# Kernel optimization log

Hardware: AMD Instinct MI355X
Metric: run time of the kernel (lower is better)

The kernel has to match this reference:

```python
import jax, jax.numpy as jnp
import numpy as np

N_MED = 100000   # len(medicine_it): nodes in the single hyperedge
VOCAB = 200000   # medicine vocab (rows of both embedding tables)
C_IN = 256
C_OUT = 256


def setup_inputs() -> dict:
    key = jax.random.key(0)
    k1, k2, k3, k4, k5 = jax.random.split(key, 5)
    return {
        "medicine_it": jax.random.randint(k1, (N_MED,), 0, VOCAB),
        "m_embeddings": jax.random.normal(k2, (VOCAB, C_IN), dtype=jnp.float32),
        "pretrained_weight": jax.random.normal(k3, (VOCAB, C_OUT), dtype=jnp.float32),
        "W": jax.random.normal(k4, (C_OUT, C_IN), dtype=jnp.float32) / np.sqrt(C_IN).astype(np.float32),
        "bias": jax.random.normal(k5, (C_OUT,), dtype=jnp.float32) * 0.01,
    }


def reference(medicine_it, m_embeddings, pretrained_weight, W, bias):
    # --- forward(): gather medicine rows, HypergraphConv with ONE hyperedge ---
    x = m_embeddings[medicine_it]                 # [N, C_in]  row gather
    xw = x @ W.T                                  # [N, C_out] lin (bias added after propagation, as in PyG)
    n = xw.shape[0]
    # Single hyperedge containing all N nodes: edge degree B = N, node degree D = 1.
    # edge_feat = B^{-1} H^T (X W^T);  node_out = D^{-1} H edge_feat + bias (same for all nodes)
    edge_feat = jnp.sum(xw, axis=0) / jnp.asarray(n, xw.dtype)   # [C_out]
    med_node_feature = edge_feat[None, :] + bias                 # [1, C_out], identical per node
    # --- output(): sum_i pretrained[m_i] + sum_i representation[i] ---
    embedding_pretrained = jnp.sum(pretrained_weight[medicine_it], axis=0, keepdims=True)  # [1, C_out]
    embedding_trained = jnp.asarray(n, xw.dtype) * med_node_feature                        # [1, C_out]
    return (embedding_pretrained + embedding_trained)[None, :, :]  # [1, 1, C_out]
```

## Files before the change

kernel.cpp:

```cpp
#include <hip/hip_runtime.h>


#define NCOPY 16

__device__ inline void fma4(float4& acc, float w, const float4& v) {
    acc.x = fmaf(w, v.x, acc.x);
    acc.y = fmaf(w, v.y, acc.y);
    acc.z = fmaf(w, v.z, acc.z);
    acc.w = fmaf(w, v.w, acc.w);
}

__global__ __launch_bounds__(256) void hist_kernel(
    const int* __restrict__ idx, int* __restrict__ counts, int n)
{
    int i = blockIdx.x * blockDim.x + threadIdx.x;
    const int stride = gridDim.x * blockDim.x;
    for (; i < n; i += stride) atomicAdd(&counts[idx[i]], 1);
}

__global__ __launch_bounds__(256) void scan_kernel(
    const int* __restrict__ counts,
    const float* __restrict__ memb,
    const float* __restrict__ pre,
    float* __restrict__ acc,
    int vocab)
{
    const int lane = threadIdx.x & 63;
    const int wid  = (blockIdx.x * blockDim.x + threadIdx.x) >> 6;
    const int base = wid * 64;

    float4 accS = make_float4(0.f, 0.f, 0.f, 0.f);
    float4 accP = make_float4(0.f, 0.f, 0.f, 0.f);

    if (base < vocab) {
        int c = 0;
        if (base + lane < vocab) c = counts[base + lane];
        const float cf = (float)c;
        unsigned long long m = __ballot(c != 0);

        while (m) {
            const int k1 = __ffsll(m) - 1;  m &= m - 1;
            const float w1 = __shfl(cf, k1, 64);
            const float4 a1 = reinterpret_cast<const float4*>(memb + (size_t)(base + k1) * 256)[lane];
            const float4 b1 = reinterpret_cast<const float4*>(pre  + (size_t)(base + k1) * 256)[lane];
            if (m) {
                const int k2 = __ffsll(m) - 1;  m &= m - 1;
                const float w2 = __shfl(cf, k2, 64);
                const float4 a2 = reinterpret_cast<const float4*>(memb + (size_t)(base + k2) * 256)[lane];
                const float4 b2 = reinterpret_cast<const float4*>(pre  + (size_t)(base + k2) * 256)[lane];
                fma4(accS, w1, a1); fma4(accP, w1, b1);
                fma4(accS, w2, a2); fma4(accP, w2, b2);
            } else {
                fma4(accS, w1, a1); fma4(accP, w1, b1);
            }
        }
    }

    __shared__ float sS[256];
    __shared__ float sP[256];
    sS[threadIdx.x] = 0.f;
    sP[threadIdx.x] = 0.f;
    __syncthreads();

    const int ch = lane * 4;
    atomicAdd(&sS[ch + 0], accS.x); atomicAdd(&sS[ch + 1], accS.y);
    atomicAdd(&sS[ch + 2], accS.z); atomicAdd(&sS[ch + 3], accS.w);
    atomicAdd(&sP[ch + 0], accP.x); atomicAdd(&sP[ch + 1], accP.y);
    atomicAdd(&sP[ch + 2], accP.z); atomicAdd(&sP[ch + 3], accP.w);
    __syncthreads();

    float* myacc = acc + (size_t)(blockIdx.x & (NCOPY - 1)) * 512;
    atomicAdd(&myacc[threadIdx.x],       sS[threadIdx.x]);
    atomicAdd(&myacc[256 + threadIdx.x], sP[threadIdx.x]);
}

__global__ __launch_bounds__(256) void gather_sum_kernel(
    const int* __restrict__ idx,
    const float* __restrict__ memb,
    const float* __restrict__ pre,
    float* __restrict__ acc,
    int n)
{
    const int lane = threadIdx.x & 63;
    const int wave = threadIdx.x >> 6;
    const int globalWave = blockIdx.x * 4 + wave;
    const int totalWaves = gridDim.x * 4;

    float4 accS = make_float4(0.f, 0.f, 0.f, 0.f);
    float4 accP = make_float4(0.f, 0.f, 0.f, 0.f);

    for (int i = globalWave; i < n; i += totalWaves) {
        const int r = idx[i];
        const float4 a = reinterpret_cast<const float4*>(memb + (size_t)r * 256)[lane];
        const float4 b = reinterpret_cast<const float4*>(pre  + (size_t)r * 256)[lane];
        accS.x += a.x; accS.y += a.y; accS.z += a.z; accS.w += a.w;
        accP.x += b.x; accP.y += b.y; accP.z += b.z; accP.w += b.w;
    }

    __shared__ float sS[256];
    __shared__ float sP[256];
    sS[threadIdx.x] = 0.f;
    sP[threadIdx.x] = 0.f;
    __syncthreads();
    const int ch = lane * 4;
    atomicAdd(&sS[ch + 0], accS.x); atomicAdd(&sS[ch + 1], accS.y);
    atomicAdd(&sS[ch + 2], accS.z); atomicAdd(&sS[ch + 3], accS.w);
    atomicAdd(&sP[ch + 0], accP.x); atomicAdd(&sP[ch + 1], accP.y);
    atomicAdd(&sP[ch + 2], accP.z); atomicAdd(&sP[ch + 3], accP.w);
    __syncthreads();
    float* myacc = acc + (size_t)(blockIdx.x & (NCOPY - 1)) * 512;
    atomicAdd(&myacc[threadIdx.x],       sS[threadIdx.x]);
    atomicAdd(&myacc[256 + threadIdx.x], sP[threadIdx.x]);
}

__global__ __launch_bounds__(256) void finish_kernel(
    const float* __restrict__ acc,
    const float* __restrict__ W,
    const float* __restrict__ bias,
    float* __restrict__ out,
    float nf)
{
    const int c = blockIdx.x;
    const int t = threadIdx.x;

    float s_t = 0.f;
    #pragma unroll
    for (int cp = 0; cp < NCOPY; ++cp) s_t += acc[cp * 512 + t];

    float v = W[(size_t)c * 256 + t] * s_t;
    for (int off = 32; off > 0; off >>= 1)
        v += __shfl_down(v, off, 64);

    __shared__ float part[4];
    if ((t & 63) == 0) part[t >> 6] = v;
    __syncthreads();

    if (t == 0) {
        float p_c = 0.f;
        #pragma unroll
        for (int cp = 0; cp < NCOPY; ++cp) p_c += acc[cp * 512 + 256 + c];
        out[c] = (part[0] + part[1] + part[2] + part[3]) + p_c + nf * bias[c];
    }
}

extern "C" void kernel_launch(void* const* d_in, const int* in_sizes, int n_in,
                              void* d_out, int out_size, void* d_ws, size_t ws_size,
                              hipStream_t stream)
{
    const int*   idx  = (const int*)d_in[0];
    const float* memb = (const float*)d_in[1];
    const float* pre  = (const float*)d_in[2];
    const float* W    = (const float*)d_in[3];
    const float* bias = (const float*)d_in[4];
    float* out = (float*)d_out;

    const int n     = in_sizes[0];
    const int vocab = in_sizes[1] / 256;

    const size_t countsBytes = (size_t)vocab * sizeof(int);
    const size_t accBytes    = (size_t)NCOPY * 512 * sizeof(float);

    if (ws_size >= countsBytes + accBytes) {
        int*   counts = (int*)d_ws;
        float* acc    = (float*)((char*)d_ws + countsBytes);

        hipMemsetAsync(d_ws, 0, countsBytes + accBytes, stream);
        hist_kernel<<<400, 256, 0, stream>>>(idx, counts, n);

        const int waves  = (vocab + 63) / 64;
        const int blocks = (waves + 3) / 4;
        scan_kernel<<<blocks, 256, 0, stream>>>(counts, memb, pre, acc, vocab);
        finish_kernel<<<256, 256, 0, stream>>>(acc, W, bias, out, (float)n);
    } else {
        float* acc = (float*)d_ws;
        hipMemsetAsync(d_ws, 0, accBytes, stream);
        gather_sum_kernel<<<512, 256, 0, stream>>>(idx, memb, pre, acc, n);
        finish_kernel<<<256, 256, 0, stream>>>(acc, W, bias, out, (float)n);
    }
}
```

Measured before the change: 53.89 us.

## Fuse finish into scan via last-block pattern and compact nonzero rows in LDS

```diff
diff --git a/kernel.cpp b/kernel.cpp
--- a/kernel.cpp
+++ b/kernel.cpp
@@ -1,59 +1,61 @@
 #include <hip/hip_runtime.h>
 
 
+typedef float f4 __attribute__((ext_vector_type(4)));
+
 #define NCOPY 16
-
-__device__ inline void fma4(float4& acc, float w, const float4& v) {
-    acc.x = fmaf(w, v.x, acc.x);
-    acc.y = fmaf(w, v.y, acc.y);
-    acc.z = fmaf(w, v.z, acc.z);
-    acc.w = fmaf(w, v.w, acc.w);
-}
 
 __global__ __launch_bounds__(256) void hist_kernel(
     const int* __restrict__ idx, int* __restrict__ counts, int n)
 {
-    int i = blockIdx.x * blockDim.x + threadIdx.x;
-    const int stride = gridDim.x * blockDim.x;
-    for (; i < n; i += stride) atomicAdd(&counts[idx[i]], 1);
-}
-
-__global__ __launch_bounds__(256) void scan_kernel(
+    const int i = blockIdx.x * blockDim.x + threadIdx.x;
+    if (i < n) atomicAdd(&counts[idx[i]], 1);
+}
+
+__global__ __launch_bounds__(256) void scan_finish_kernel(
     const int* __restrict__ counts,
     const float* __restrict__ memb,
     const float* __restrict__ pre,
     float* __restrict__ acc,
-    int vocab)
+    int* __restrict__ done,
+    const float* __restrict__ W,
+    const float* __restrict__ bias,
+    float* __restrict__ out,
+    int vocab, float nf, int nblocks)
 {
     const int lane = threadIdx.x & 63;
+    const int wv   = threadIdx.x >> 6;
     const int wid  = (blockIdx.x * blockDim.x + threadIdx.x) >> 6;
     const int base = wid * 64;
 
-    float4 accS = make_float4(0.f, 0.f, 0.f, 0.f);
-    float4 accP = make_float4(0.f, 0.f, 0.f, 0.f);
-
-    if (base < vocab) {
-        int c = 0;
-        if (base + lane < vocab) c = counts[base + lane];
-        const float cf = (float)c;
-        unsigned long long m = __ballot(c != 0);
-
-        while (m) {
-            const int k1 = __ffsll(m) - 1;  m &= m - 1;
-            const float w1 = __shfl(cf, k1, 64);
-            const float4 a1 = reinterpret_cast<const float4*>(memb + (size_t)(base + k1) * 256)[lane];
-            const float4 b1 = reinterpret_cast<const float4*>(pre  + (size_t)(base + k1) * 256)[lane];
-            if (m) {
-                const int k2 = __ffsll(m) - 1;  m &= m - 1;
-                const float w2 = __shfl(cf, k2, 64);
-                const float4 a2 = reinterpret_cast<const float4*>(memb + (size_t)(base + k2) * 256)[lane];
-                const float4 b2 = reinterpret_cast<const float4*>(pre  + (size_t)(base + k2) * 256)[lane];
-                fma4(accS, w1, a1); fma4(accP, w1, b1);
-                fma4(accS, w2, a2); fma4(accP, w2, b2);
-            } else {
-                fma4(accS, w1, a1); fma4(accP, w1, b1);
-            }
-        }
+    __shared__ int   sRow[4][64];
+    __shared__ float sWt [4][64];
+
+    int c = 0;
+    if (base + lane < vocab) c = counts[base + lane];
+    const unsigned long long mm = __ballot(c != 0);
+    const int nv = __popcll(mm);
+    if (c != 0) {
+        const int pos = __popcll(mm & ((1ull << lane) - 1));
+        sRow[wv][pos] = lane;
+        sWt [wv][pos] = (float)c;
+    }
+    __syncthreads();
+
+    f4 accS = {0.f, 0.f, 0.f, 0.f};
+    f4 accP = {0.f, 0.f, 0.f, 0.f};
+
+    const f4* mrow = reinterpret_cast<const f4*>(memb) + (size_t)base * 64 + lane;
+    const f4* prow = reinterpret_cast<const f4*>(pre)  + (size_t)base * 64 + lane;
+
+    #pragma unroll 4
+    for (int j = 0; j < nv; ++j) {
+        const int   k = sRow[wv][j];
+        const float w = sWt [wv][j];
+        const f4 a = __builtin_nontemporal_load(mrow + (size_t)k * 64);
+        const f4 b = __builtin_nontemporal_load(prow + (size_t)k * 64);
+        accS += a * w;
+        accP += b * w;
     }
 
     __shared__ float sS[256];
@@ -72,6 +74,34 @@
     float* myacc = acc + (size_t)(blockIdx.x & (NCOPY - 1)) * 512;
     atomicAdd(&myacc[threadIdx.x],       sS[threadIdx.x]);
     atomicAdd(&myacc[256 + threadIdx.x], sP[threadIdx.x]);
+
+    __shared__ int lastFlag;
+    if (threadIdx.x == 0) {
+        __threadfence();
+        lastFlag = (atomicAdd(done, 1) == nblocks - 1);
+    }
+    __syncthreads();
+    if (!lastFlag) return;
+    __threadfence();
+
+    const int t = threadIdx.x;
+    float s_t = 0.f, p_t = 0.f;
+    #pragma unroll
+    for (int cp = 0; cp < NCOPY; ++cp) {
+        s_t += acc[cp * 512 + t];
+        p_t += acc[cp * 512 + 256 + t];
+    }
+
+    __shared__ float sVec[256];
+    sVec[t] = s_t;
+    __syncthreads();
+
+    float v = 0.f;
+    #pragma unroll 8
+    for (int k = 0; k < 256; ++k)
+        v = fmaf(W[(size_t)t * 256 + k], sVec[k], v);
+
+    out[t] = v + p_t + nf * bias[t];
 }
 
 __global__ __launch_bounds__(256) void gather_sum_kernel(
@@ -86,15 +116,14 @@
     const int globalWave = blockIdx.x * 4 + wave;
     const int totalWaves = gridDim.x * 4;
 
-    float4 accS = make_float4(0.f, 0.f, 0.f, 0.f);
-    float4 accP = make_float4(0.f, 0.f, 0.f, 0.f);
+    f4 accS = {0.f,0.f,0.f,0.f};
+    f4 accP = {0.f,0.f,0.f,0.f};
 
     for (int i = globalWave; i < n; i += totalWaves) {
         const int r = idx[i];
-        const float4 a = reinterpret_cast<const float4*>(memb + (size_t)r * 256)[lane];
-        const float4 b = reinterpret_cast<const float4*>(pre  + (size_t)r * 256)[lane];
-        accS.x += a.x; accS.y += a.y; accS.z += a.z; accS.w += a.w;
-        accP.x += b.x; accP.y += b.y; accP.z += b.z; accP.w += b.w;
+        const f4 a = reinterpret_cast<const f4*>(memb + (size_t)r * 256)[lane];
+        const f4 b = reinterpret_cast<const f4*>(pre  + (size_t)r * 256)[lane];
+        accS += a; accP += b;
     }
 
     __shared__ float sS[256];
@@ -160,17 +189,19 @@
     const size_t countsBytes = (size_t)vocab * sizeof(int);
     const size_t accBytes    = (size_t)NCOPY * 512 * sizeof(float);
 
-    if (ws_size >= countsBytes + accBytes) {
+    if (ws_size >= countsBytes + accBytes + 64) {
         int*   counts = (int*)d_ws;
         float* acc    = (float*)((char*)d_ws + countsBytes);
-
-        hipMemsetAsync(d_ws, 0, countsBytes + accBytes, stream);
-        hist_kernel<<<400, 256, 0, stream>>>(idx, counts, n);
+        int*   done   = (int*)((char*)d_ws + countsBytes + accBytes);
+
+        hipMemsetAsync(d_ws, 0, countsBytes + accBytes + 64, stream);
+
+        hist_kernel<<<(n + 255) / 256, 256, 0, stream>>>(idx, counts, n);
 
         const int waves  = (vocab + 63) / 64;
         const int blocks = (waves + 3) / 4;
-        scan_kernel<<<blocks, 256, 0, stream>>>(counts, memb, pre, acc, vocab);
-        finish_kernel<<<256, 256, 0, stream>>>(acc, W, bias, out, (float)n);
+        scan_finish_kernel<<<blocks, 256, 0, stream>>>(
+            counts, memb, pre, acc, done, W, bias, out, vocab, (float)n, blocks);
     } else {
         float* acc = (float*)d_ws;
         hipMemsetAsync(d_ws, 0, accBytes, stream);
```

Result: slower. 88.31 us (+63.9%).
